# Kernel tuning notes

Measured on AMD Instinct MI355X. Metric: run time of the kernel, lower is better.

Reference implementation:

```python
import jax, jax.numpy as jnp
import numpy as np
import math

N_HEADS = 8
N_LEVELS = 3
N_POINTS = 4
D_MODEL = 128
D_HEAD = D_MODEL // N_HEADS  # 16
SHAPES = [(128, 128), (64, 64), (32, 32)]  # (H, W) per level
N = 1
LQ = 6400  # 80x80 BEV queries


def _xavier(k, shape):
    lim = math.sqrt(6.0 / (shape[0] + shape[1]))
    return jax.random.uniform(k, shape, jnp.float32, -lim, lim)


def _grid_init_bias():
    # faithful to _reset_parameters: per-head directional bias, scaled per point
    thetas = np.arange(N_HEADS, dtype=np.float32) * (2.0 * np.pi / N_HEADS)
    grid = np.stack([np.cos(thetas), np.sin(thetas)], -1)
    grid = grid / np.abs(grid).max(-1, keepdims=True)
    grid = np.tile(grid.reshape(N_HEADS, 1, 1, 2), (1, N_LEVELS, N_POINTS, 1))
    grid = grid * (np.arange(N_POINTS, dtype=np.float32) + 1.0).reshape(1, 1, N_POINTS, 1)
    return jnp.asarray(grid.reshape(-1), jnp.float32)


def setup_inputs() -> dict:
    key = jax.random.key(0)
    ks = jax.random.split(key, 12)
    query = jax.random.normal(ks[0], (N, LQ, D_MODEL), jnp.float32)
    reference_points = jax.random.uniform(ks[1], (N, LQ, N_LEVELS, 2), jnp.float32)
    feat0 = jax.random.normal(ks[2], (N, 128, SHAPES[0][0], SHAPES[0][1]), jnp.float32)
    feat1 = jax.random.normal(ks[3], (N, 128, SHAPES[1][0], SHAPES[1][1]), jnp.float32)
    feat2 = jax.random.normal(ks[4], (N, 64, SHAPES[2][0], SHAPES[2][1]), jnp.float32)
    input_spatial_shapes = jnp.array(SHAPES, jnp.int32)
    # torch inits weight to 0; use small random so grads wrt W_off are exercised
    W_off = jax.random.normal(ks[5], (N_HEADS * N_LEVELS * N_POINTS * 2, D_MODEL), jnp.float32) * 0.01
    b_off = _grid_init_bias()
    Wk0 = _xavier(ks[6], (128, 128)); bk0 = jnp.zeros((128,), jnp.float32)
    Wk1 = _xavier(ks[7], (128, 128)); bk1 = jnp.zeros((128,), jnp.float32)
    Wk2 = _xavier(ks[8], (128, 64)); bk2 = jnp.zeros((128,), jnp.float32)
    W_out = _xavier(ks[9], (128, 128)); b_out = jnp.zeros((128,), jnp.float32)
    return {
        'query': query, 'reference_points': reference_points,
        'feat0': feat0, 'feat1': feat1, 'feat2': feat2,
        'input_spatial_shapes': input_spatial_shapes,
        'W_off': W_off, 'b_off': b_off,
        'Wk0': Wk0, 'bk0': bk0, 'Wk1': Wk1, 'bk1': bk1, 'Wk2': Wk2, 'bk2': bk2,
        'W_out': W_out, 'b_out': b_out,
    }


def _bilinear_sample(feat, loc):
    # feat: (N, C, H, W); loc: (N, S, 2) in [0,1]; grid_sample align_corners=False, zero padding
    n, c, h, w = feat.shape
    x = loc[..., 0] * w - 0.5
    y = loc[..., 1] * h - 0.5
    x0 = jnp.floor(x); y0 = jnp.floor(y)
    wx = x - x0; wy = y - y0  # (N, S)
    x0i = x0.astype(jnp.int32); y0i = y0.astype(jnp.int32)
    flat = feat.reshape(n, c, h * w)

    def gather(xi, yi):
        valid = (xi >= 0) & (xi < w) & (yi >= 0) & (yi < h)
        idx = jnp.clip(yi, 0, h - 1) * w + jnp.clip(xi, 0, w - 1)
        v = jnp.take_along_axis(flat, idx[:, None, :], axis=2)  # (N, C, S)
        return v * valid[:, None, :].astype(feat.dtype)

    out = (gather(x0i, y0i) * ((1 - wx) * (1 - wy))[:, None, :]
           + gather(x0i + 1, y0i) * (wx * (1 - wy))[:, None, :]
           + gather(x0i, y0i + 1) * ((1 - wx) * wy)[:, None, :]
           + gather(x0i + 1, y0i + 1) * (wx * wy)[:, None, :])
    return out  # (N, C, S)


def _forward(query, reference_points, feat0, feat1, feat2, input_spatial_shapes,
             W_off, b_off, Wk0, bk0, Wk1, bk1, Wk2, bk2, W_out, b_out):
    n, lq, _ = query.shape
    off = (query @ W_off.T + b_off).reshape(n, lq, N_HEADS, N_LEVELS, N_POINTS, 2)
    shp = input_spatial_shapes.astype(query.dtype)
    norm = jnp.stack([shp[:, 1], shp[:, 0]], -1)  # (L, 2) = (W, H)
    # sampling locations in [0,1]: (N, Lq, H, L, P, 2)
    loc = reference_points[:, :, None, :, None, :] + off / norm[None, None, None, :, None, :]
    qh = query.reshape(n, lq, N_HEADS, D_HEAD)
    feats = [feat0, feat1, feat2]
    Wks = [Wk0, Wk1, Wk2]
    bks = [bk0, bk1, bk2]
    logits, vals = [], []
    for l in range(N_LEVELS):
        c = feats[l].shape[1]
        ll = loc[:, :, :, l, :, :].reshape(n, lq * N_HEADS * N_POINTS, 2)
        s = _bilinear_sample(feats[l], ll)  # (N, C, Lq*H*P)
        s = s.reshape(n, c, lq, N_HEADS, N_POINTS).transpose(0, 2, 3, 4, 1)  # (N, Lq, H, P, C)
        # per-head key projection: head h uses its 16-dim slice of the 128-d projection
        k = jnp.einsum('nqhpc,hdc->nqhpd', s, Wks[l].reshape(N_HEADS, D_HEAD, c))
        k = k + bks[l].reshape(N_HEADS, D_HEAD)[None, None, :, None, :]
        logits.append(jnp.einsum('nqhd,nqhpd->nqhp', qh, k))
        vals.append(k)
    logits = jnp.stack(logits, 3)  # (N, Lq, H, L, P)
    vals = jnp.stack(vals, 3)      # (N, Lq, H, L, P, D_HEAD)
    scale = 1.0 / math.sqrt(D_HEAD)
    attn = jax.nn.softmax((logits * scale).reshape(n, lq, N_HEADS, N_LEVELS * N_POINTS), -1)
    attn = attn.reshape(n, lq, N_HEADS, N_LEVELS, N_POINTS)
    out = jnp.einsum('nqhlp,nqhlpd->nqhd', attn, vals).reshape(n, lq, D_MODEL)
    out = out @ W_out.T + b_out
    return out.transpose(1, 0, 2)  # (Lq, N, C) per output.permute(1,0,2)


def reference(query, reference_points, feat0, feat1, feat2, input_spatial_shapes,
              W_off, b_off, Wk0, bk0, Wk1, bk1, Wk2, bk2, W_out, b_out):
    return _forward(query, reference_points, feat0, feat1, feat2, input_spatial_shapes,
                    W_off, b_off, Wk0, bk0, Wk1, bk1, Wk2, bk2, W_out, b_out)
```

## Files before the change

kernel.cpp:

```cpp
#include <hip/hip_runtime.h>
#include <hip/hip_bf16.h>
#include <math.h>

#define LQ 6400


template<int C>
__device__ __forceinline__ void proj_body(
    float* __restrict__ smem,
    const float* __restrict__ feat, const float* __restrict__ Wk,
    __hip_bfloat16* __restrict__ P, int HW, int local)
{
    constexpr int CI4 = C / 4;
    float* wk_sh = smem;
    float* f_sh  = smem + 64 * C;
    int pblk = local >> 1;
    int half = local & 1;
    int cbase = half * 64;
    int p0 = pblk * 64;
    int tid = threadIdx.x;

    for (int idx = tid; idx < 64 * CI4; idx += 256) {
        int rl = idx / CI4;
        int ci4 = idx % CI4;
        float4 v = *reinterpret_cast<const float4*>(&Wk[(cbase + rl) * C + ci4 * 4]);
        *reinterpret_cast<float4*>(&wk_sh[rl * C + ((ci4 ^ (rl & (CI4 - 1))) << 2)]) = v;
    }
    for (int idx = tid; idx < C * 16; idx += 256) {
        int ci = idx >> 4;
        int pp4 = idx & 15;
        float4 v = *reinterpret_cast<const float4*>(&feat[ci * HW + p0 + pp4 * 4]);
        *reinterpret_cast<float4*>(&f_sh[ci * 64 + pp4 * 4]) = v;
    }
    __syncthreads();

    int c0 = tid & 31;
    int pg = tid >> 5;
    const int sw = c0 & (CI4 - 1);
    float acc[2][8];
    #pragma unroll
    for (int k = 0; k < 2; ++k)
        #pragma unroll
        for (int j = 0; j < 8; ++j) acc[k][j] = 0.f;

    #pragma unroll 4
    for (int ci4 = 0; ci4 < CI4; ++ci4) {
        float4 A0 = *reinterpret_cast<const float4*>(&wk_sh[c0 * C + ((ci4 ^ sw) << 2)]);
        float4 A1 = *reinterpret_cast<const float4*>(&wk_sh[(c0 + 32) * C + ((ci4 ^ sw) << 2)]);
        float a0v[4] = {A0.x, A0.y, A0.z, A0.w};
        float a1v[4] = {A1.x, A1.y, A1.z, A1.w};
        #pragma unroll
        for (int jj = 0; jj < 4; ++jj) {
            int ci = ci4 * 4 + jj;
            float4 Blo = *reinterpret_cast<const float4*>(&f_sh[ci * 64 + pg * 8]);
            float4 Bhi = *reinterpret_cast<const float4*>(&f_sh[ci * 64 + pg * 8 + 4]);
            float bv[8] = {Blo.x, Blo.y, Blo.z, Blo.w, Bhi.x, Bhi.y, Bhi.z, Bhi.w};
            #pragma unroll
            for (int j = 0; j < 8; ++j) {
                acc[0][j] = fmaf(a0v[jj], bv[j], acc[0][j]);
                acc[1][j] = fmaf(a1v[jj], bv[j], acc[1][j]);
            }
        }
    }
    #pragma unroll
    for (int k = 0; k < 2; ++k) {
        int co = cbase + c0 + 32 * k;
        #pragma unroll
        for (int j = 0; j < 8; ++j)
            P[(size_t)(p0 + pg * 8 + j) * 128 + co] = __float2bfloat16(acc[k][j]);
    }
}

__device__ __forceinline__ void off_body(
    float* __restrict__ smem,
    const float* __restrict__ query, const float* __restrict__ W_off,
    const float* __restrict__ b_off, float* __restrict__ offv, int local)
{
    float* w_sh = smem;
    float* q_sh = smem + 96 * 128;
    int qblk = local >> 1;
    int half = local & 1;
    int rbase = half * 96;
    int q0 = qblk * 32;
    int tid = threadIdx.x;

    for (int idx = tid; idx < 96 * 32; idx += 256) {
        int rl = idx >> 5;
        int ci4 = idx & 31;
        float4 v = *reinterpret_cast<const float4*>(&W_off[(rbase + rl) * 128 + ci4 * 4]);
        *reinterpret_cast<float4*>(&w_sh[rl * 128 + ((ci4 ^ (rl & 31)) << 2)]) = v;
    }
    for (int idx = tid; idx < 32 * 32; idx += 256) {
        int qq = idx >> 5;
        int ci4 = idx & 31;
        *reinterpret_cast<float4*>(&q_sh[qq * 128 + ci4 * 4]) =
            *reinterpret_cast<const float4*>(&query[(q0 + qq) * 128 + ci4 * 4]);
    }
    __syncthreads();

    int c0 = tid & 31;
    int qg = tid >> 5;
    float acc[3][4];
    #pragma unroll
    for (int k = 0; k < 3; ++k)
        #pragma unroll
        for (int j = 0; j < 4; ++j) acc[k][j] = 0.f;

    #pragma unroll 4
    for (int ci4 = 0; ci4 < 32; ++ci4) {
        float4 A[3];
        #pragma unroll
        for (int k = 0; k < 3; ++k)
            A[k] = *reinterpret_cast<const float4*>(&w_sh[(c0 + 32 * k) * 128 + ((ci4 ^ c0) << 2)]);
        #pragma unroll
        for (int j = 0; j < 4; ++j) {
            float4 B = *reinterpret_cast<const float4*>(&q_sh[(qg * 4 + j) * 128 + ci4 * 4]);
            #pragma unroll
            for (int k = 0; k < 3; ++k) {
                acc[k][j] = fmaf(A[k].x, B.x, acc[k][j]);
                acc[k][j] = fmaf(A[k].y, B.y, acc[k][j]);
                acc[k][j] = fmaf(A[k].z, B.z, acc[k][j]);
                acc[k][j] = fmaf(A[k].w, B.w, acc[k][j]);
            }
        }
    }
    #pragma unroll
    for (int k = 0; k < 3; ++k) {
        int r = rbase + c0 + 32 * k;
        float bias = b_off[r];
        #pragma unroll
        for (int j = 0; j < 4; ++j)
            offv[(q0 + qg * 4 + j) * 192 + r] = acc[k][j] + bias;
    }
}

__global__ __launch_bounds__(256) void prep_kernel(
    const float* __restrict__ feat0, const float* __restrict__ feat1,
    const float* __restrict__ feat2,
    const float* __restrict__ Wk0, const float* __restrict__ Wk1,
    const float* __restrict__ Wk2,
    __hip_bfloat16* __restrict__ P0, __hip_bfloat16* __restrict__ P1,
    __hip_bfloat16* __restrict__ P2,
    const float* __restrict__ query, const float* __restrict__ W_off,
    const float* __restrict__ b_off, float* __restrict__ offv)
{
    __shared__ __align__(16) float smem[16384];
    int b = blockIdx.x;
    if (b < 512) {
        proj_body<128>(smem, feat0, Wk0, P0, 16384, b);
    } else if (b < 640) {
        proj_body<128>(smem, feat1, Wk1, P1, 4096, b - 512);
    } else if (b < 672) {
        proj_body<64>(smem, feat2, Wk2, P2, 1024, b - 640);
    } else {
        off_body(smem, query, W_off, b_off, offv, b - 672);
    }
}

__global__ __launch_bounds__(128) void attn3_kernel(
    const float* __restrict__ query, const float* __restrict__ ref,
    const float* __restrict__ offv,
    const __hip_bfloat16* __restrict__ P0, const __hip_bfloat16* __restrict__ P1,
    const __hip_bfloat16* __restrict__ P2,
    const float* __restrict__ bk0, const float* __restrict__ bk1,
    const float* __restrict__ bk2,
    float* __restrict__ hout)
{
    __shared__ float q_sh[128];
    __shared__ float off_sh[192];
    __shared__ float ref_sh[6];
    __shared__ float bias_sh[3][128];
    __shared__ float logit_sh[96];
    __shared__ __align__(16) float k_sh[8 * 196];
    int q = blockIdx.x;
    int tid = threadIdx.x;
    q_sh[tid] = query[q * 128 + tid];
    bias_sh[0][tid] = bk0[tid];
    bias_sh[1][tid] = bk1[tid];
    bias_sh[2][tid] = bk2[tid];
    off_sh[tid] = offv[q * 192 + tid];
    if (tid < 64) off_sh[128 + tid] = offv[q * 192 + 128 + tid];
    if (tid < 6) ref_sh[tid] = ref[q * 6 + tid];
    __syncthreads();

    const int grp = tid >> 4;
    const int d = tid & 15;
    const int c = d >> 2;
    const int quad = d & 3;
    const int dxl = c & 1;
    const int dyl = c >> 1;

    uint2 raw[12];
    float wcv[12];
    #pragma unroll
    for (int it = 0; it < 12; ++it) {
        int s = it * 8 + grp;
        int h = (s * 171) >> 11;
        int lp = s - h * 12;
        int l = lp >> 2;
        int W = 128 >> l;
        float ox = off_sh[2 * s];
        float oy = off_sh[2 * s + 1];
        float x = fmaf(ref_sh[2 * l], (float)W, ox) - 0.5f;
        float y = fmaf(ref_sh[2 * l + 1], (float)W, oy) - 0.5f;
        float x0f = floorf(x), y0f = floorf(y);
        float wx = x - x0f, wy = y - y0f;
        int xs = (int)x0f + dxl;
        int ys = (int)y0f + dyl;
        float m = (xs >= 0 && xs < W && ys >= 0 && ys < W) ? 1.f : 0.f;
        float fx = dxl ? wx : 1.f - wx;
        float fy = dyl ? wy : 1.f - wy;
        wcv[it] = fx * fy * m;
        int xc = min(max(xs, 0), W - 1);
        int yc = min(max(ys, 0), W - 1);
        const __hip_bfloat16* P = (l == 0) ? P0 : ((l == 1) ? P1 : P2);
        size_t idx = (size_t)(yc * W + xc) * 128 + h * 16 + quad * 4;
        raw[it] = *reinterpret_cast<const uint2*>(P + idx);
    }

    #pragma unroll
    for (int it = 0; it < 12; ++it) {
        int s = it * 8 + grp;
        int h = (s * 171) >> 11;
        int lp = s - h * 12;
        int l = lp >> 2;
        unsigned a = raw[it].x, bb = raw[it].y;
        float w = wcv[it];
        float k0 = w * __uint_as_float(a << 16);
        float k1 = w * __uint_as_float(a & 0xffff0000u);
        float k2 = w * __uint_as_float(bb << 16);
        float k3 = w * __uint_as_float(bb & 0xffff0000u);
        k0 += __shfl_xor(k0, 4); k1 += __shfl_xor(k1, 4);
        k2 += __shfl_xor(k2, 4); k3 += __shfl_xor(k3, 4);
        k0 += __shfl_xor(k0, 8); k1 += __shfl_xor(k1, 8);
        k2 += __shfl_xor(k2, 8); k3 += __shfl_xor(k3, 8);
        int co4 = h * 16 + quad * 4;
        k0 += bias_sh[l][co4 + 0];
        k1 += bias_sh[l][co4 + 1];
        k2 += bias_sh[l][co4 + 2];
        k3 += bias_sh[l][co4 + 3];
        float lg = q_sh[co4] * k0;
        lg = fmaf(q_sh[co4 + 1], k1, lg);
        lg = fmaf(q_sh[co4 + 2], k2, lg);
        lg = fmaf(q_sh[co4 + 3], k3, lg);
        lg += __shfl_xor(lg, 1);
        lg += __shfl_xor(lg, 2);
        if (d < 4) {
            float4 kv = make_float4(k0, k1, k2, k3);
            *reinterpret_cast<float4*>(&k_sh[h * 196 + lp * 16 + d * 4]) = kv;
        }
        if (d == 0) logit_sh[h * 12 + lp] = lg;
    }
    __syncthreads();

    int h2 = tid >> 4, dd = tid & 15;
    float m = -1e30f;
    #pragma unroll
    for (int j = 0; j < 12; ++j) m = fmaxf(m, logit_sh[h2 * 12 + j]);
    float ssum = 0.f, o = 0.f;
    #pragma unroll
    for (int j = 0; j < 12; ++j) {
        float e = __expf(0.25f * (logit_sh[h2 * 12 + j] - m));
        ssum += e;
        o = fmaf(e, k_sh[h2 * 196 + j * 16 + dd], o);
    }
    hout[q * 128 + tid] = o / ssum;
}

__global__ __launch_bounds__(256) void outp2_kernel(
    const float* __restrict__ hin, const float* __restrict__ W_out,
    const float* __restrict__ b_out, float* __restrict__ out)
{
    __shared__ __align__(16) float w_sh[64 * 128];
    __shared__ __align__(16) float q_sh[64 * 128];
    int b = blockIdx.x;
    int qblk = b >> 1;
    int half = b & 1;
    int rbase = half * 64;
    int q0 = qblk * 64;
    int tid = threadIdx.x;

    for (int idx = tid; idx < 64 * 32; idx += 256) {
        int rl = idx >> 5;
        int ci4 = idx & 31;
        float4 v = *reinterpret_cast<const float4*>(&W_out[(rbase + rl) * 128 + ci4 * 4]);
        *reinterpret_cast<float4*>(&w_sh[rl * 128 + ((ci4 ^ (rl & 31)) << 2)]) = v;
    }
    for (int idx = tid; idx < 64 * 32; idx += 256) {
        int qq = idx >> 5;
        int ci4 = idx & 31;
        *reinterpret_cast<float4*>(&q_sh[qq * 128 + ci4 * 4]) =
            *reinterpret_cast<const float4*>(&hin[(q0 + qq) * 128 + ci4 * 4]);
    }
    __syncthreads();

    int c0 = tid & 31;
    int qg = tid >> 5;
    float acc[2][8];
    #pragma unroll
    for (int k = 0; k < 2; ++k)
        #pragma unroll
        for (int j = 0; j < 8; ++j) acc[k][j] = 0.f;

    #pragma unroll 4
    for (int ci4 = 0; ci4 < 32; ++ci4) {
        float4 A0 = *reinterpret_cast<const float4*>(&w_sh[c0 * 128 + ((ci4 ^ c0) << 2)]);
        float4 A1 = *reinterpret_cast<const float4*>(&w_sh[(c0 + 32) * 128 + ((ci4 ^ c0) << 2)]);
        #pragma unroll
        for (int j = 0; j < 8; ++j) {
            float4 B = *reinterpret_cast<const float4*>(&q_sh[(qg * 8 + j) * 128 + ci4 * 4]);
            acc[0][j] = fmaf(A0.x, B.x, acc[0][j]);
            acc[0][j] = fmaf(A0.y, B.y, acc[0][j]);
            acc[0][j] = fmaf(A0.z, B.z, acc[0][j]);
            acc[0][j] = fmaf(A0.w, B.w, acc[0][j]);
            acc[1][j] = fmaf(A1.x, B.x, acc[1][j]);
            acc[1][j] = fmaf(A1.y, B.y, acc[1][j]);
            acc[1][j] = fmaf(A1.z, B.z, acc[1][j]);
            acc[1][j] = fmaf(A1.w, B.w, acc[1][j]);
        }
    }
    #pragma unroll
    for (int k = 0; k < 2; ++k) {
        int r = rbase + c0 + 32 * k;
        float bias = b_out[r];
        #pragma unroll
        for (int j = 0; j < 8; ++j)
            out[(q0 + qg * 8 + j) * 128 + r] = acc[k][j] + bias;
    }
}

extern "C" void kernel_launch(void* const* d_in, const int* in_sizes, int n_in,
                              void* d_out, int out_size, void* d_ws, size_t ws_size,
                              hipStream_t stream) {
    const float* query = (const float*)d_in[0];
    const float* ref   = (const float*)d_in[1];
    const float* feat0 = (const float*)d_in[2];
    const float* feat1 = (const float*)d_in[3];
    const float* feat2 = (const float*)d_in[4];
    const float* W_off = (const float*)d_in[6];
    const float* b_off = (const float*)d_in[7];
    const float* Wk0   = (const float*)d_in[8];
    const float* bk0   = (const float*)d_in[9];
    const float* Wk1   = (const float*)d_in[10];
    const float* bk1   = (const float*)d_in[11];
    const float* Wk2   = (const float*)d_in[12];
    const float* bk2   = (const float*)d_in[13];
    const float* W_out = (const float*)d_in[14];
    const float* b_out = (const float*)d_in[15];
    float* out = (float*)d_out;

    __hip_bfloat16* P0 = (__hip_bfloat16*)d_ws;
    __hip_bfloat16* P1 = P0 + 16384 * 128;
    __hip_bfloat16* P2 = P1 + 4096 * 128;
    float* offv = (float*)(P2 + 1024 * 128);
    float* hout = offv + 6400 * 192;

    hipLaunchKernelGGL(prep_kernel, dim3(1072), dim3(256), 0, stream,
                       feat0, feat1, feat2, Wk0, Wk1, Wk2, P0, P1, P2,
                       query, W_off, b_off, offv);
    hipLaunchKernelGGL(attn3_kernel, dim3(6400), dim3(128), 0, stream,
                       query, ref, offv, P0, P1, P2, bk0, bk1, bk2, hout);
    hipLaunchKernelGGL(outp2_kernel, dim3(200), dim3(256), 0, stream,
                       hout, W_out, b_out, out);
}
```

Measured before the change: 157.9 us.

## Use bf16 MFMA for key and offset projections, head-major key layout

```diff
diff --git a/kernel.cpp b/kernel.cpp
--- a/kernel.cpp
+++ b/kernel.cpp
@@ -2,139 +2,128 @@
 #include <hip/hip_bf16.h>
 #include <math.h>
 
-#define LQ 6400
-
+typedef __attribute__((ext_vector_type(8))) short bf16x8;
+typedef __attribute__((ext_vector_type(4))) float f32x4;
+
+__device__ __forceinline__ unsigned f2bfu(float f) {
+    __hip_bfloat16 b = __float2bfloat16(f);
+    return (unsigned)*reinterpret_cast<unsigned short*>(&b);
+}
+
+__device__ __forceinline__ bf16x8 cvt8(float4 a, float4 b) {
+    bf16x8 r;
+    r[0] = (short)f2bfu(a.x); r[1] = (short)f2bfu(a.y);
+    r[2] = (short)f2bfu(a.z); r[3] = (short)f2bfu(a.w);
+    r[4] = (short)f2bfu(b.x); r[5] = (short)f2bfu(b.y);
+    r[6] = (short)f2bfu(b.z); r[7] = (short)f2bfu(b.w);
+    return r;
+}
 
 template<int C>
-__device__ __forceinline__ void proj_body(
-    float* __restrict__ smem,
-    const float* __restrict__ feat, const float* __restrict__ Wk,
-    __hip_bfloat16* __restrict__ P, int HW, int local)
-{
-    constexpr int CI4 = C / 4;
-    float* wk_sh = smem;
-    float* f_sh  = smem + 64 * C;
-    int pblk = local >> 1;
-    int half = local & 1;
-    int cbase = half * 64;
-    int p0 = pblk * 64;
-    int tid = threadIdx.x;
-
-    for (int idx = tid; idx < 64 * CI4; idx += 256) {
-        int rl = idx / CI4;
-        int ci4 = idx % CI4;
-        float4 v = *reinterpret_cast<const float4*>(&Wk[(cbase + rl) * C + ci4 * 4]);
-        *reinterpret_cast<float4*>(&wk_sh[rl * C + ((ci4 ^ (rl & (CI4 - 1))) << 2)]) = v;
-    }
-    for (int idx = tid; idx < C * 16; idx += 256) {
-        int ci = idx >> 4;
-        int pp4 = idx & 15;
-        float4 v = *reinterpret_cast<const float4*>(&feat[ci * HW + p0 + pp4 * 4]);
-        *reinterpret_cast<float4*>(&f_sh[ci * 64 + pp4 * 4]) = v;
+__device__ __forceinline__ void proj_mfma(
+    unsigned short* lds, const float* __restrict__ feat,
+    const float* __restrict__ Wk, __hip_bfloat16* __restrict__ P,
+    int HW, int pblk)
+{
+    constexpr int GR = C / 8;
+    constexpr int KK = C / 32;
+    const int tid = threadIdx.x;
+    const int p0 = pblk * 128;
+
+    for (int u = tid; u < (C / 2) * 32; u += 256) {
+        int cip = u >> 5;
+        int p4 = (u & 31) << 2;
+        int ci = cip << 1;
+        float4 lo = *reinterpret_cast<const float4*>(feat + (size_t)ci * HW + p0 + p4);
+        float4 hi = *reinterpret_cast<const float4*>(feat + (size_t)(ci + 1) * HW + p0 + p4);
+        float lov[4] = {lo.x, lo.y, lo.z, lo.w};
+        float hiv[4] = {hi.x, hi.y, hi.z, hi.w};
+        int g = ci >> 3;
+        #pragma unroll
+        for (int j = 0; j < 4; ++j) {
+            int pix = p4 + j;
+            int gs = g ^ (pix & (GR - 1));
+            unsigned pack = f2bfu(lov[j]) | (f2bfu(hiv[j]) << 16);
+            *reinterpret_cast<unsigned*>(lds + pix * C + gs * 8 + (ci & 7)) = pack;
+        }
     }
     __syncthreads();
 
-    int c0 = tid & 31;
-    int pg = tid >> 5;
-    const int sw = c0 & (CI4 - 1);
-    float acc[2][8];
-    #pragma unroll
-    for (int k = 0; k < 2; ++k)
-        #pragma unroll
-        for (int j = 0; j < 8; ++j) acc[k][j] = 0.f;
-
-    #pragma unroll 4
-    for (int ci4 = 0; ci4 < CI4; ++ci4) {
-        float4 A0 = *reinterpret_cast<const float4*>(&wk_sh[c0 * C + ((ci4 ^ sw) << 2)]);
-        float4 A1 = *reinterpret_cast<const float4*>(&wk_sh[(c0 + 32) * C + ((ci4 ^ sw) << 2)]);
-        float a0v[4] = {A0.x, A0.y, A0.z, A0.w};
-        float a1v[4] = {A1.x, A1.y, A1.z, A1.w};
-        #pragma unroll
-        for (int jj = 0; jj < 4; ++jj) {
-            int ci = ci4 * 4 + jj;
-            float4 Blo = *reinterpret_cast<const float4*>(&f_sh[ci * 64 + pg * 8]);
-            float4 Bhi = *reinterpret_cast<const float4*>(&f_sh[ci * 64 + pg * 8 + 4]);
-            float bv[8] = {Blo.x, Blo.y, Blo.z, Blo.w, Bhi.x, Bhi.y, Bhi.z, Bhi.w};
+    const int wave = tid >> 6, lane = tid & 63;
+    const int col = lane & 15, g4 = lane >> 4;
+
+    bf16x8 bfrag[2][KK];
+    #pragma unroll
+    for (int st = 0; st < 2; ++st) {
+        int pix = (wave * 2 + st) * 16 + col;
+        #pragma unroll
+        for (int kk = 0; kk < KK; ++kk) {
+            int gs = (kk * 4 + g4) ^ (pix & (GR - 1));
+            bfrag[st][kk] = *reinterpret_cast<const bf16x8*>(lds + pix * C + gs * 8);
+        }
+    }
+    #pragma unroll
+    for (int h = 0; h < 8; ++h) {
+        bf16x8 afrag[KK];
+        #pragma unroll
+        for (int kk = 0; kk < KK; ++kk) {
+            const float* wp = Wk + (size_t)(h * 16 + col) * C + kk * 32 + g4 * 8;
+            afrag[kk] = cvt8(*reinterpret_cast<const float4*>(wp),
+                             *reinterpret_cast<const float4*>(wp + 4));
+        }
+        #pragma unroll
+        for (int st = 0; st < 2; ++st) {
+            f32x4 acc = {0.f, 0.f, 0.f, 0.f};
             #pragma unroll
-            for (int j = 0; j < 8; ++j) {
-                acc[0][j] = fmaf(a0v[jj], bv[j], acc[0][j]);
-                acc[1][j] = fmaf(a1v[jj], bv[j], acc[1][j]);
-            }
-        }
-    }
-    #pragma unroll
-    for (int k = 0; k < 2; ++k) {
-        int co = cbase + c0 + 32 * k;
-        #pragma unroll
-        for (int j = 0; j < 8; ++j)
-            P[(size_t)(p0 + pg * 8 + j) * 128 + co] = __float2bfloat16(acc[k][j]);
-    }
-}
-
-__device__ __forceinline__ void off_body(
-    float* __restrict__ smem,
+            for (int kk = 0; kk < KK; ++kk)
+                acc = __builtin_amdgcn_mfma_f32_16x16x32_bf16(afrag[kk], bfrag[st][kk], acc, 0, 0, 0);
+            int pix = p0 + (wave * 2 + st) * 16 + col;
+            unsigned lo = f2bfu(acc[0]) | (f2bfu(acc[1]) << 16);
+            unsigned hi = f2bfu(acc[2]) | (f2bfu(acc[3]) << 16);
+            uint2 od = make_uint2(lo, hi);
+            *reinterpret_cast<uint2*>(reinterpret_cast<char*>(P) +
+                (size_t)(h * HW + pix) * 32 + g4 * 8) = od;
+        }
+    }
+}
+
+__device__ __forceinline__ void off_mfma(
     const float* __restrict__ query, const float* __restrict__ W_off,
-    const float* __restrict__ b_off, float* __restrict__ offv, int local)
-{
-    float* w_sh = smem;
-    float* q_sh = smem + 96 * 128;
-    int qblk = local >> 1;
-    int half = local & 1;
-    int rbase = half * 96;
-    int q0 = qblk * 32;
-    int tid = threadIdx.x;
-
-    for (int idx = tid; idx < 96 * 32; idx += 256) {
-        int rl = idx >> 5;
-        int ci4 = idx & 31;
-        float4 v = *reinterpret_cast<const float4*>(&W_off[(rbase + rl) * 128 + ci4 * 4]);
-        *reinterpret_cast<float4*>(&w_sh[rl * 128 + ((ci4 ^ (rl & 31)) << 2)]) = v;
-    }
-    for (int idx = tid; idx < 32 * 32; idx += 256) {
-        int qq = idx >> 5;
-        int ci4 = idx & 31;
-        *reinterpret_cast<float4*>(&q_sh[qq * 128 + ci4 * 4]) =
-            *reinterpret_cast<const float4*>(&query[(q0 + qq) * 128 + ci4 * 4]);
-    }
-    __syncthreads();
-
-    int c0 = tid & 31;
-    int qg = tid >> 5;
-    float acc[3][4];
-    #pragma unroll
-    for (int k = 0; k < 3; ++k)
-        #pragma unroll
-        for (int j = 0; j < 4; ++j) acc[k][j] = 0.f;
-
-    #pragma unroll 4
-    for (int ci4 = 0; ci4 < 32; ++ci4) {
-        float4 A[3];
-        #pragma unroll
-        for (int k = 0; k < 3; ++k)
-            A[k] = *reinterpret_cast<const float4*>(&w_sh[(c0 + 32 * k) * 128 + ((ci4 ^ c0) << 2)]);
-        #pragma unroll
-        for (int j = 0; j < 4; ++j) {
-            float4 B = *reinterpret_cast<const float4*>(&q_sh[(qg * 4 + j) * 128 + ci4 * 4]);
-            #pragma unroll
-            for (int k = 0; k < 3; ++k) {
-                acc[k][j] = fmaf(A[k].x, B.x, acc[k][j]);
-                acc[k][j] = fmaf(A[k].y, B.y, acc[k][j]);
-                acc[k][j] = fmaf(A[k].z, B.z, acc[k][j]);
-                acc[k][j] = fmaf(A[k].w, B.w, acc[k][j]);
-            }
-        }
-    }
-    #pragma unroll
-    for (int k = 0; k < 3; ++k) {
-        int r = rbase + c0 + 32 * k;
-        float bias = b_off[r];
-        #pragma unroll
-        for (int j = 0; j < 4; ++j)
-            offv[(q0 + qg * 4 + j) * 192 + r] = acc[k][j] + bias;
-    }
-}
-
-__global__ __launch_bounds__(256) void prep_kernel(
+    const float* __restrict__ b_off, float* __restrict__ offv, int qblk)
+{
+    const int tid = threadIdx.x;
+    const int wave = tid >> 6, lane = tid & 63;
+    const int col = lane & 15, g4 = lane >> 4;
+    const int q = qblk * 64 + wave * 16 + col;
+
+    bf16x8 bfrag[4];
+    #pragma unroll
+    for (int kk = 0; kk < 4; ++kk) {
+        const float* qp = query + (size_t)q * 128 + kk * 32 + g4 * 8;
+        bfrag[kk] = cvt8(*reinterpret_cast<const float4*>(qp),
+                         *reinterpret_cast<const float4*>(qp + 4));
+    }
+    #pragma unroll
+    for (int mt = 0; mt < 12; ++mt) {
+        bf16x8 afrag[4];
+        #pragma unroll
+        for (int kk = 0; kk < 4; ++kk) {
+            const float* wp = W_off + (size_t)(mt * 16 + col) * 128 + kk * 32 + g4 * 8;
+            afrag[kk] = cvt8(*reinterpret_cast<const float4*>(wp),
+                             *reinterpret_cast<const float4*>(wp + 4));
+        }
+        f32x4 acc = {0.f, 0.f, 0.f, 0.f};
+        #pragma unroll
+        for (int kk = 0; kk < 4; ++kk)
+            acc = __builtin_amdgcn_mfma_f32_16x16x32_bf16(afrag[kk], bfrag[kk], acc, 0, 0, 0);
+        float4 bias = *reinterpret_cast<const float4*>(b_off + mt * 16 + g4 * 4);
+        float4 o = make_float4(acc[0] + bias.x, acc[1] + bias.y,
+                               acc[2] + bias.z, acc[3] + bias.w);
+        *reinterpret_cast<float4*>(offv + (size_t)q * 192 + mt * 16 + g4 * 4) = o;
+    }
+}
+
+__global__ __launch_bounds__(256) void prep3_kernel(
     const float* __restrict__ feat0, const float* __restrict__ feat1,
     const float* __restrict__ feat2,
     const float* __restrict__ Wk0, const float* __restrict__ Wk1,
@@ -144,20 +133,15 @@
     const float* __restrict__ query, const float* __restrict__ W_off,
     const float* __restrict__ b_off, float* __restrict__ offv)
 {
-    __shared__ __align__(16) float smem[16384];
+    __shared__ __align__(16) unsigned short lds[128 * 128];
     int b = blockIdx.x;
-    if (b < 512) {
-        proj_body<128>(smem, feat0, Wk0, P0, 16384, b);
-    } else if (b < 640) {
-        proj_body<128>(smem, feat1, Wk1, P1, 4096, b - 512);
-    } else if (b < 672) {
-        proj_body<64>(smem, feat2, Wk2, P2, 1024, b - 640);
-    } else {
-        off_body(smem, query, W_off, b_off, offv, b - 672);
-    }
-}
-
-__global__ __launch_bounds__(128) void attn3_kernel(
+    if (b < 128)      proj_mfma<128>(lds, feat0, Wk0, P0, 16384, b);
+    else if (b < 160) proj_mfma<128>(lds, feat1, Wk1, P1, 4096, b - 128);
+    else if (b < 168) proj_mfma<64>(lds, feat2, Wk2, P2, 1024, b - 160);
+    else              off_mfma(query, W_off, b_off, offv, b - 168);
+}
+
+__global__ __launch_bounds__(128) void attn4_kernel(
     const float* __restrict__ query, const float* __restrict__ ref,
     const float* __restrict__ offv,
     const __hip_bfloat16* __restrict__ P0, const __hip_bfloat16* __restrict__ P1,
@@ -166,90 +150,97 @@
     const float* __restrict__ bk2,
     float* __restrict__ hout)
 {
-    __shared__ float q_sh[128];
-    __shared__ float off_sh[192];
-    __shared__ float ref_sh[6];
-    __shared__ float bias_sh[3][128];
+    __shared__ __align__(16) float q_sh[128];
+    __shared__ __align__(16) float bias_sh[3][128];
     __shared__ float logit_sh[96];
-    __shared__ __align__(16) float k_sh[8 * 196];
+    __shared__ __align__(16) float k_sh[96 * 20];
+    __shared__ __align__(16) unsigned gaddr[96][4];
+    __shared__ __align__(16) float gw[96][4];
     int q = blockIdx.x;
     int tid = threadIdx.x;
     q_sh[tid] = query[q * 128 + tid];
     bias_sh[0][tid] = bk0[tid];
     bias_sh[1][tid] = bk1[tid];
     bias_sh[2][tid] = bk2[tid];
-    off_sh[tid] = offv[q * 192 + tid];
-    if (tid < 64) off_sh[128 + tid] = offv[q * 192 + 128 + tid];
-    if (tid < 6) ref_sh[tid] = ref[q * 6 + tid];
-    __syncthreads();
-
-    const int grp = tid >> 4;
-    const int d = tid & 15;
-    const int c = d >> 2;
-    const int quad = d & 3;
-    const int dxl = c & 1;
-    const int dyl = c >> 1;
-
-    uint2 raw[12];
-    float wcv[12];
-    #pragma unroll
-    for (int it = 0; it < 12; ++it) {
-        int s = it * 8 + grp;
+    if (tid < 96) {
+        int s = tid;
         int h = (s * 171) >> 11;
         int lp = s - h * 12;
         int l = lp >> 2;
         int W = 128 >> l;
-        float ox = off_sh[2 * s];
-        float oy = off_sh[2 * s + 1];
-        float x = fmaf(ref_sh[2 * l], (float)W, ox) - 0.5f;
-        float y = fmaf(ref_sh[2 * l + 1], (float)W, oy) - 0.5f;
+        float ox = offv[q * 192 + 2 * s];
+        float oy = offv[q * 192 + 2 * s + 1];
+        float x = fmaf(ref[q * 6 + 2 * l], (float)W, ox) - 0.5f;
+        float y = fmaf(ref[q * 6 + 2 * l + 1], (float)W, oy) - 0.5f;
         float x0f = floorf(x), y0f = floorf(y);
         float wx = x - x0f, wy = y - y0f;
-        int xs = (int)x0f + dxl;
-        int ys = (int)y0f + dyl;
-        float m = (xs >= 0 && xs < W && ys >= 0 && ys < W) ? 1.f : 0.f;
-        float fx = dxl ? wx : 1.f - wx;
-        float fy = dyl ? wy : 1.f - wy;
-        wcv[it] = fx * fy * m;
-        int xc = min(max(xs, 0), W - 1);
-        int yc = min(max(ys, 0), W - 1);
-        const __hip_bfloat16* P = (l == 0) ? P0 : ((l == 1) ? P1 : P2);
-        size_t idx = (size_t)(yc * W + xc) * 128 + h * 16 + quad * 4;
-        raw[it] = *reinterpret_cast<const uint2*>(P + idx);
-    }
-
-    #pragma unroll
-    for (int it = 0; it < 12; ++it) {
-        int s = it * 8 + grp;
+        int x0 = (int)x0f, y0 = (int)y0f;
+        int x1 = x0 + 1, y1 = y0 + 1;
+        float mx0 = (x0 >= 0 && x0 < W) ? 1.f : 0.f;
+        float mx1 = (x1 >= 0 && x1 < W) ? 1.f : 0.f;
+        float my0 = (y0 >= 0 && y0 < W) ? 1.f : 0.f;
+        float my1 = (y1 >= 0 && y1 < W) ? 1.f : 0.f;
+        int xc0 = min(max(x0, 0), W - 1), xc1 = min(max(x1, 0), W - 1);
+        int yc0 = min(max(y0, 0), W - 1), yc1 = min(max(y1, 0), W - 1);
+        unsigned pb = (unsigned)(h * W * W) * 32u;
+        gaddr[s][0] = pb + (unsigned)(yc0 * W + xc0) * 32u;
+        gaddr[s][1] = pb + (unsigned)(yc0 * W + xc1) * 32u;
+        gaddr[s][2] = pb + (unsigned)(yc1 * W + xc0) * 32u;
+        gaddr[s][3] = pb + (unsigned)(yc1 * W + xc1) * 32u;
+        gw[s][0] = (1.f - wx) * (1.f - wy) * mx0 * my0;
+        gw[s][1] = wx * (1.f - wy) * mx1 * my0;
+        gw[s][2] = (1.f - wx) * wy * mx0 * my1;
+        gw[s][3] = wx * wy * mx1 * my1;
+    }
+    __syncthreads();
+
+    const int quad = tid & 3;
+    uint2 raw[3][4];
+    float4 wv[3];
+    int hs[3], lps[3], lvs[3];
+    #pragma unroll
+    for (int it = 0; it < 3; ++it) {
+        int s = it * 32 + (tid >> 2);
         int h = (s * 171) >> 11;
         int lp = s - h * 12;
         int l = lp >> 2;
-        unsigned a = raw[it].x, bb = raw[it].y;
-        float w = wcv[it];
-        float k0 = w * __uint_as_float(a << 16);
-        float k1 = w * __uint_as_float(a & 0xffff0000u);
-        float k2 = w * __uint_as_float(bb << 16);
-        float k3 = w * __uint_as_float(bb & 0xffff0000u);
-        k0 += __shfl_xor(k0, 4); k1 += __shfl_xor(k1, 4);
-        k2 += __shfl_xor(k2, 4); k3 += __shfl_xor(k3, 4);
-        k0 += __shfl_xor(k0, 8); k1 += __shfl_xor(k1, 8);
-        k2 += __shfl_xor(k2, 8); k3 += __shfl_xor(k3, 8);
-        int co4 = h * 16 + quad * 4;
-        k0 += bias_sh[l][co4 + 0];
-        k1 += bias_sh[l][co4 + 1];
-        k2 += bias_sh[l][co4 + 2];
-        k3 += bias_sh[l][co4 + 3];
-        float lg = q_sh[co4] * k0;
-        lg = fmaf(q_sh[co4 + 1], k1, lg);
-        lg = fmaf(q_sh[co4 + 2], k2, lg);
-        lg = fmaf(q_sh[co4 + 3], k3, lg);
+        hs[it] = h; lps[it] = lp; lvs[it] = l;
+        uint4 av = *reinterpret_cast<const uint4*>(&gaddr[s][0]);
+        wv[it] = *reinterpret_cast<const float4*>(&gw[s][0]);
+        const char* base = ((l == 0) ? (const char*)P0 :
+                            (l == 1) ? (const char*)P1 : (const char*)P2) + quad * 8;
+        raw[it][0] = *reinterpret_cast<const uint2*>(base + av.x);
+        raw[it][1] = *reinterpret_cast<const uint2*>(base + av.y);
+        raw[it][2] = *reinterpret_cast<const uint2*>(base + av.z);
+        raw[it][3] = *reinterpret_cast<const uint2*>(base + av.w);
+    }
+    #pragma unroll
+    for (int it = 0; it < 3; ++it) {
+        int s = it * 32 + (tid >> 2);
+        int h = hs[it], l = lvs[it];
+        float k0 = 0.f, k1 = 0.f, k2 = 0.f, k3 = 0.f;
+        float wc[4] = {wv[it].x, wv[it].y, wv[it].z, wv[it].w};
+        #pragma unroll
+        for (int cnr = 0; cnr < 4; ++cnr) {
+            unsigned a = raw[it][cnr].x, b2 = raw[it][cnr].y;
+            float w = wc[cnr];
+            k0 = fmaf(w, __uint_as_float(a << 16), k0);
+            k1 = fmaf(w, __uint_as_float(a & 0xffff0000u), k1);
+            k2 = fmaf(w, __uint_as_float(b2 << 16), k2);
+            k3 = fmaf(w, __uint_as_float(b2 & 0xffff0000u), k3);
+        }
+        int co = h * 16 + quad * 4;
+        float4 bias = *reinterpret_cast<const float4*>(&bias_sh[l][co]);
+        k0 += bias.x; k1 += bias.y; k2 += bias.z; k3 += bias.w;
+        float4 qv = *reinterpret_cast<const float4*>(&q_sh[co]);
+        float lg = k0 * qv.x;
+        lg = fmaf(k1, qv.y, lg);
+        lg = fmaf(k2, qv.z, lg);
+        lg = fmaf(k3, qv.w, lg);
         lg += __shfl_xor(lg, 1);
         lg += __shfl_xor(lg, 2);
-        if (d < 4) {
-            float4 kv = make_float4(k0, k1, k2, k3);
-            *reinterpret_cast<float4*>(&k_sh[h * 196 + lp * 16 + d * 4]) = kv;
-        }
-        if (d == 0) logit_sh[h * 12 + lp] = lg;
+        *reinterpret_cast<float4*>(&k_sh[s * 20 + quad * 4]) = make_float4(k0, k1, k2, k3);
+        if (quad == 0) logit_sh[s] = lg;
     }
     __syncthreads();
 
@@ -262,7 +253,7 @@
     for (int j = 0; j < 12; ++j) {
         float e = __expf(0.25f * (logit_sh[h2 * 12 + j] - m));
         ssum += e;
-        o = fmaf(e, k_sh[h2 * 196 + j * 16 + dd], o);
+        o = fmaf(e, k_sh[(h2 * 12 + j) * 20 + dd], o);
     }
     hout[q * 128 + tid] = o / ssum;
 }
@@ -350,15 +341,15 @@
     float* out = (float*)d_out;
 
     __hip_bfloat16* P0 = (__hip_bfloat16*)d_ws;
-    __hip_bfloat16* P1 = P0 + 16384 * 128;
-    __hip_bfloat16* P2 = P1 + 4096 * 128;
-    float* offv = (float*)(P2 + 1024 * 128);
+    __hip_bfloat16* P1 = P0 + 8 * 16384 * 16;
+    __hip_bfloat16* P2 = P1 + 8 * 4096 * 16;
+    float* offv = (float*)(P2 + 8 * 1024 * 16);
     float* hout = offv + 6400 * 192;
 
-    hipLaunchKernelGGL(prep_kernel, dim3(1072), dim3(256), 0, stream,
+    hipLaunchKernelGGL(prep3_kernel, dim3(268), dim3(256), 0, stream,
                        feat0, feat1, feat2, Wk0, Wk1, Wk2, P0, P1, P2,
                        query, W_off, b_off, offv);
-    hipLaunchKernelGGL(attn3_kernel, dim3(6400), dim3(128), 0, stream,
+    hipLaunchKernelGGL(attn4_kernel, dim3(6400), dim3(128), 0, stream,
                        query, ref, offv, P0, P1, P2, bk0, bk1, bk2, hout);
     hipLaunchKernelGGL(outp2_kernel, dim3(200), dim3(256), 0, stream,
                        hout, W_out, b_out, out);
```

Measured after the change: 133.5 us. 15.5% less time.
